# Kernel tuning notes

Measured on AMD Instinct MI355X. Metric: run time of the kernel, lower is better.

Reference implementation:

```python
import jax, jax.numpy as jnp
import numpy as np

N, E, F, H, C, G = 50000, 800000, 128, 1, 64, 256
NEG_SLOPE = 0.2


def _seg_softmax(e, seg, n):
    # numerically-stable softmax over edges grouped by target node
    m = jax.ops.segment_max(e, seg, num_segments=n)
    ex = jnp.exp(e - m[seg])
    s = jax.ops.segment_sum(ex, seg, num_segments=n)
    return ex / (s[seg] + 1e-16)


def _gatv2(x, src, dst, wl, bl, wr, br, att, bo, n):
    # GATv2Conv (PyG semantics): lin_l on source x_j, lin_r on target x_i
    xl = (x @ wl.T + bl).reshape(n, H, C)
    xr = (x @ wr.T + br).reshape(n, H, C)
    s = xl[src] + xr[dst]                      # [E, H, C]
    e = jnp.sum(jax.nn.leaky_relu(s, NEG_SLOPE) * att, axis=-1)  # [E, H]
    alpha = _seg_softmax(e, dst, n)
    out = jax.ops.segment_sum(alpha[..., None] * xl[src], dst, num_segments=n)
    return out.reshape(n, H * C) + bo


def setup_inputs() -> dict:
    key = jax.random.key(0)
    ks = jax.random.split(key, 24)
    d = {}
    d['x'] = jax.random.normal(ks[0], (N, F), dtype=jnp.float32)
    d['edge_index'] = jax.random.randint(ks[1], (2, E), 0, N)
    d['batch_idx'] = jnp.sort(jax.random.randint(ks[2], (N,), 0, G))
    sc = 0.1
    # conv1: in=F, out=C
    d['wl1'] = jax.random.normal(ks[3], (H * C, F)) * sc
    d['bl1'] = jnp.zeros((H * C,), jnp.float32)
    d['wr1'] = jax.random.normal(ks[4], (H * C, F)) * sc
    d['br1'] = jnp.zeros((H * C,), jnp.float32)
    d['att1'] = jax.random.normal(ks[5], (H, C)) * sc
    d['bo1'] = jnp.zeros((H * C,), jnp.float32)
    # conv2, conv3: in=H*C, out=C
    d['wl2'] = jax.random.normal(ks[6], (H * C, H * C)) * sc
    d['bl2'] = jnp.zeros((H * C,), jnp.float32)
    d['wr2'] = jax.random.normal(ks[7], (H * C, H * C)) * sc
    d['br2'] = jnp.zeros((H * C,), jnp.float32)
    d['att2'] = jax.random.normal(ks[8], (H, C)) * sc
    d['bo2'] = jnp.zeros((H * C,), jnp.float32)
    d['wl3'] = jax.random.normal(ks[9], (H * C, H * C)) * sc
    d['bl3'] = jnp.zeros((H * C,), jnp.float32)
    d['wr3'] = jax.random.normal(ks[10], (H * C, H * C)) * sc
    d['br3'] = jnp.zeros((H * C,), jnp.float32)
    d['att3'] = jax.random.normal(ks[11], (H, C)) * sc
    d['bo3'] = jnp.zeros((H * C,), jnp.float32)
    # heads
    d['lin1_w'] = jax.random.normal(ks[12], (C, 3 * H * C)) * sc
    d['lin1_b'] = jnp.zeros((C,), jnp.float32)
    d['pred_w'] = jax.random.normal(ks[13], (C, C)) * sc
    d['pred_b'] = jnp.zeros((C,), jnp.float32)
    d['cls_w'] = jax.random.normal(ks[14], (2, C)) * sc
    d['cls_b'] = jnp.zeros((2,), jnp.float32)
    return d


def reference(x, edge_index, batch_idx, wl1, bl1, wr1, br1, att1, bo1,
              wl2, bl2, wr2, br2, att2, bo2, wl3, bl3, wr3, br3, att3, bo3,
              lin1_w, lin1_b, pred_w, pred_b, cls_w, cls_b):
    # add self-loops (GATv2Conv default add_self_loops=True)
    loop = jnp.arange(N, dtype=edge_index.dtype)
    src = jnp.concatenate([edge_index[0], loop])
    dst = jnp.concatenate([edge_index[1], loop])
    x1 = jax.nn.relu(_gatv2(x, src, dst, wl1, bl1, wr1, br1, att1, bo1, N))
    x2 = jax.nn.relu(_gatv2(x1, src, dst, wl2, bl2, wr2, br2, att2, bo2, N))
    x3 = jax.nn.relu(_gatv2(x2, src, dst, wl3, bl3, wr3, br3, att3, bo3, N))
    h = jax.nn.relu(jnp.concatenate([x1, x2, x3], axis=1) @ lin1_w.T + lin1_b)
    g = jax.ops.segment_sum(h, batch_idx, num_segments=G)  # global_add_pool
    emb = jax.nn.relu(g @ pred_w.T + pred_b)                # pred_layer
    out = emb @ cls_w.T + cls_b                             # cls_layer
    return out
```

## Files before the change

kernel.cpp:

```cpp
#include <hip/hip_runtime.h>
#include <hip/hip_bf16.h>

#define N_NODES 50000
#define N_EDGES 800000
#define FDIM 128
#define CDIM 64
#define NGRAPH 256
#define LRELU_SLOPE 0.2f
#define SCAN_NB ((N_NODES + 1023) / 1024)
#define NBUCK ((N_NODES + 255) / 256)
#define BCAP 5120
#define ABLK 400
#define EPB ((N_EDGES + ABLK - 1) / ABLK)
#define NDBIN 64

typedef unsigned short ushort_t;
typedef unsigned int uint_t;
typedef __attribute__((ext_vector_type(8))) short short8v;
typedef __attribute__((ext_vector_type(4))) float float4v;

__device__ __forceinline__ ushort_t f2bf(float f) {
    uint_t u = __float_as_uint(f);
    u += 0x7FFFu + ((u >> 16) & 1u);
    return (ushort_t)(u >> 16);
}
__device__ __forceinline__ float bf2f(ushort_t u) {
    return __uint_as_float(((uint_t)u) << 16);
}

__device__ __forceinline__ float fast_exp2(float x) {
    return __builtin_amdgcn_exp2f(x);
}

__device__ __forceinline__ int wave_incl_scan(int v, int lane) {
#pragma unroll
    for (int off = 1; off < 64; off <<= 1) {
        int t = __shfl_up(v, off);
        if (lane >= off) v += t;
    }
    return v;
}

__device__ __forceinline__ float wave_sum(float v) {
#pragma unroll
    for (int off = 32; off >= 1; off >>= 1) v += __shfl_xor(v, off);
    return v;
}

__global__ void k_bucket(const int* __restrict__ src, const int* __restrict__ dst,
                         int* __restrict__ bcnt, int2* __restrict__ stage) {
    __shared__ int lhist[NBUCK];
    __shared__ int lbase[NBUCK];
    __shared__ int lcur[NBUCK];
    int tid = threadIdx.x;
    int e0 = blockIdx.x * EPB;
    int e1 = min(e0 + EPB, N_EDGES);
    for (int t = tid; t < NBUCK; t += 256) { lhist[t] = 0; lcur[t] = 0; }
    __syncthreads();
    for (int e = e0 + tid; e < e1; e += 256)
        atomicAdd(&lhist[dst[e] >> 8], 1);
    __syncthreads();
    for (int t = tid; t < NBUCK; t += 256)
        lbase[t] = atomicAdd(&bcnt[t], lhist[t]);
    __syncthreads();
    for (int e = e0 + tid; e < e1; e += 256) {
        int s = src[e], d = dst[e];
        int b = d >> 8;
        int loff = atomicAdd(&lcur[b], 1);
        int pos = lbase[b] + loff;
        if (pos < BCAP) stage[(size_t)b * BCAP + pos] = make_int2(s, d);
    }
}

__global__ void k_hist2(const int* __restrict__ bcnt, const int2* __restrict__ stage,
                        int* __restrict__ cnt, int* __restrict__ dhist) {
    __shared__ int lcnt[256];
    __shared__ int ldh[NDBIN];
    int b = blockIdx.x;
    int tid = threadIdx.x;
    lcnt[tid] = 0;
    if (tid < NDBIN) ldh[tid] = 0;
    __syncthreads();
    int n = min(bcnt[b], BCAP);
    const int2* sp = stage + (size_t)b * BCAP;
    for (int i = tid; i < n; i += 256)
        atomicAdd(&lcnt[sp[i].y & 255], 1);
    __syncthreads();
    int node = (b << 8) + tid;
    if (node < N_NODES) {
        cnt[node] = lcnt[tid];
        atomicAdd(&ldh[min(lcnt[tid], NDBIN - 1)], 1);
    }
    __syncthreads();
    if (tid < NDBIN && ldh[tid]) atomicAdd(&dhist[tid], ldh[tid]);
}

__global__ void k_scan1(const int* __restrict__ cnt, int* __restrict__ rowptr,
                        int* __restrict__ blocksum) {
    __shared__ int wsum[16];
    int tid = threadIdx.x;
    int gid = blockIdx.x * 1024 + tid;
    int lane = tid & 63, wid = tid >> 6;
    int v = (gid < N_NODES) ? cnt[gid] : 0;
    int incl = wave_incl_scan(v, lane);
    if (lane == 63) wsum[wid] = incl;
    __syncthreads();
    if (wid == 0) {
        int wv = (lane < 16) ? wsum[lane] : 0;
        int wincl = wave_incl_scan(wv, lane);
        if (lane < 16) wsum[lane] = wincl - wv;
    }
    __syncthreads();
    int excl = incl - v + wsum[wid];
    if (gid < N_NODES) rowptr[gid] = excl;
    if (tid == 1023) blocksum[blockIdx.x] = excl + v;
}

__global__ void k_scan2(int* __restrict__ blocksum, const int* __restrict__ dhist,
                        int* __restrict__ dcur) {
    int tid = threadIdx.x;
    if (tid < 64) {
        int lane = tid;
        int v = (lane < SCAN_NB) ? blocksum[lane] : 0;
        int incl = wave_incl_scan(v, lane);
        if (lane < SCAN_NB) blocksum[lane] = incl - v;
    } else {
        int lane = tid - 64;
        int v = dhist[lane];
        int incl = wave_incl_scan(v, lane);
        dcur[lane] = incl - v;
    }
}

__global__ void k_scan3(int* __restrict__ rowptr, const int* __restrict__ blocksum,
                        int* __restrict__ cursor) {
    int tid = threadIdx.x;
    int gid = blockIdx.x * 1024 + tid;
    if (gid < N_NODES) {
        int r = rowptr[gid] + blocksum[blockIdx.x];
        rowptr[gid] = r;
        cursor[gid] = r;
    }
    if (blockIdx.x == 0 && tid == 0) rowptr[N_NODES] = N_EDGES;
}

__global__ void k_scatter2(const int* __restrict__ bcnt, const int2* __restrict__ stage,
                           int* __restrict__ cursor, int* __restrict__ csr_src) {
    int b = blockIdx.x;
    int tid = threadIdx.x;
    int n = min(bcnt[b], BCAP);
    const int2* sp = stage + (size_t)b * BCAP;
    for (int i = tid; i < n; i += 256) {
        int2 sd = sp[i];
        int pos = atomicAdd(&cursor[sd.y], 1);
        csr_src[pos] = sd.x;
    }
}

__global__ void k_dscatter(const int* __restrict__ cnt, int* __restrict__ dcur,
                           int* __restrict__ order) {
    __shared__ int lh[NDBIN], lb[NDBIN], lc[NDBIN];
    int b = blockIdx.x, tid = threadIdx.x;
    if (tid < NDBIN) { lh[tid] = 0; lc[tid] = 0; }
    __syncthreads();
    int node = b * 256 + tid;
    bool ok = node < N_NODES;
    int dg = ok ? min(cnt[node], NDBIN - 1) : 0;
    if (ok) atomicAdd(&lh[dg], 1);
    __syncthreads();
    if (tid < NDBIN) lb[tid] = lh[tid] ? atomicAdd(&dcur[tid], lh[tid]) : 0;
    __syncthreads();
    if (ok) {
        int off2 = atomicAdd(&lc[dg], 1);
        order[lb[dg] + off2] = node;
    }
}

struct WSrc {
    const float* s[7];
    int off[8];
};
__global__ void k_cvt_w(WSrc ws, ushort_t* __restrict__ hi, ushort_t* __restrict__ lo) {
    int gid = blockIdx.x * 256 + threadIdx.x;
    int stride = gridDim.x * 256;
#pragma unroll
    for (int mi = 0; mi < 7; mi++) {
        int n = ws.off[mi + 1] - ws.off[mi];
        const float* s = ws.s[mi];
        ushort_t* h = hi + ws.off[mi];
        ushort_t* l = lo + ws.off[mi];
        for (int i = gid; i < n; i += stride) {
            float f = s[i];
            ushort_t hb = f2bf(f);
            h[i] = hb;
            l[i] = f2bf(f - bf2f(hb));
        }
    }
}

template <int K, bool A_FP32>
__global__ void k_gemm_dual_mfma(const void* __restrict__ xa,
                                 const ushort_t* __restrict__ wlh, const ushort_t* __restrict__ wll,
                                 const ushort_t* __restrict__ wrh, const ushort_t* __restrict__ wrl,
                                 const float* __restrict__ bl, const float* __restrict__ br,
                                 ushort_t* __restrict__ xl, ushort_t* __restrict__ xr) {
    int tid = threadIdx.x;
    int wv = tid >> 6, lane = tid & 63;
    int m0 = blockIdx.x * 64 + wv * 16;
    if (m0 >= N_NODES) return;
    int arow = min(m0 + (lane & 15), N_NODES - 1);
    int koff = (lane >> 4) * 8;
    int wrow = lane & 15;

    float4v acc[8];
#pragma unroll
    for (int f = 0; f < 8; f++) acc[f] = (float4v)(0.f);

#pragma unroll
    for (int k0 = 0; k0 < K; k0 += 32) {
        short8v afrag;
        if (A_FP32) {
            const float* ap = (const float*)xa + (size_t)arow * K + k0 + koff;
            float4 a0 = *reinterpret_cast<const float4*>(ap);
            float4 a1 = *reinterpret_cast<const float4*>(ap + 4);
            afrag[0] = (short)f2bf(a0.x); afrag[1] = (short)f2bf(a0.y);
            afrag[2] = (short)f2bf(a0.z); afrag[3] = (short)f2bf(a0.w);
            afrag[4] = (short)f2bf(a1.x); afrag[5] = (short)f2bf(a1.y);
            afrag[6] = (short)f2bf(a1.z); afrag[7] = (short)f2bf(a1.w);
        } else {
            afrag = *reinterpret_cast<const short8v*>((const ushort_t*)xa + (size_t)arow * K + k0 + koff);
        }
#pragma unroll
        for (int f = 0; f < 8; f++) {
            const ushort_t* bh = (f < 4) ? wlh : wrh;
            const ushort_t* blo = (f < 4) ? wll : wrl;
            int row = ((f * 16 + wrow) & 63);
            size_t boff = (size_t)row * K + k0 + koff;
            short8v bfh = *reinterpret_cast<const short8v*>(bh + boff);
            short8v bfl = *reinterpret_cast<const short8v*>(blo + boff);
            acc[f] = __builtin_amdgcn_mfma_f32_16x16x32_bf16(afrag, bfh, acc[f], 0, 0, 0);
            acc[f] = __builtin_amdgcn_mfma_f32_16x16x32_bf16(afrag, bfl, acc[f], 0, 0, 0);
        }
    }

    int r0 = m0 + (lane >> 4) * 4;
#pragma unroll
    for (int f = 0; f < 8; f++) {
        int col = f * 16 + (lane & 15);
        float bias = (col < 64) ? bl[col] : br[col - 64];
        ushort_t* dstp = (col < 64) ? xl : xr;
        int c = col & 63;
#pragma unroll
        for (int j = 0; j < 4; j++) {
            int row = r0 + j;
            if (row < N_NODES) dstp[(size_t)row * 64 + c] = f2bf(acc[f][j] + bias);
        }
    }
}

__global__ void k_gemm_h_pool(const ushort_t* __restrict__ x1, const ushort_t* __restrict__ x2,
                              const ushort_t* __restrict__ x3,
                              const ushort_t* __restrict__ whi, const ushort_t* __restrict__ wlo,
                              const float* __restrict__ b, const int* __restrict__ batch,
                              float* __restrict__ g) {
    __shared__ float ht[64][65];
    int tid = threadIdx.x;
    int wv = tid >> 6, lane = tid & 63;
    int m0 = blockIdx.x * 64 + wv * 16;
    bool wactive = m0 < N_NODES;

    if (wactive) {
        int arow = min(m0 + (lane & 15), N_NODES - 1);
        int koff = (lane >> 4) * 8;
        int wrow = lane & 15;
        float4v acc[4];
#pragma unroll
        for (int f = 0; f < 4; f++) acc[f] = (float4v)(0.f);
#pragma unroll
        for (int ks = 0; ks < 6; ks++) {
            int k0 = ks * 32;
            const ushort_t* srcp = (ks < 2) ? x1 : (ks < 4 ? x2 : x3);
            int kc = k0 & 63;
            short8v afrag = *reinterpret_cast<const short8v*>(srcp + (size_t)arow * 64 + kc + koff);
#pragma unroll
            for (int f = 0; f < 4; f++) {
                size_t boff = (size_t)(f * 16 + wrow) * 192 + k0 + koff;
                short8v bfh = *reinterpret_cast<const short8v*>(whi + boff);
                short8v bfl = *reinterpret_cast<const short8v*>(wlo + boff);
                acc[f] = __builtin_amdgcn_mfma_f32_16x16x32_bf16(afrag, bfh, acc[f], 0, 0, 0);
                acc[f] = __builtin_amdgcn_mfma_f32_16x16x32_bf16(afrag, bfl, acc[f], 0, 0, 0);
            }
        }
        int r0 = wv * 16 + (lane >> 4) * 4;
#pragma unroll
        for (int f = 0; f < 4; f++) {
            int col = f * 16 + (lane & 15);
            float bias = b[col];
#pragma unroll
            for (int j = 0; j < 4; j++) {
                float o = acc[f][j] + bias;
                ht[r0 + j][col] = o > 0.f ? o : 0.f;
            }
        }
    }
    __syncthreads();

    int c = tid & 63, rr = tid >> 6;
    int blkbase = blockIdx.x * 64;
    float acc = 0.f;
    int cur = -1;
    for (int r = rr; r < 64; r += 4) {
        int node = blkbase + r;
        if (node >= N_NODES) break;
        int bb = batch[node];
        if (bb != cur) {
            if (cur >= 0) atomicAdd(&g[cur * 64 + c], acc);
            cur = bb;
            acc = 0.f;
        }
        acc += ht[r][c];
    }
    if (cur >= 0) atomicAdd(&g[cur * 64 + c], acc);
}

__global__ void k_gat(const ushort_t* __restrict__ xl, const ushort_t* __restrict__ xr,
                      const int* __restrict__ rowptr, const int* __restrict__ csr_src,
                      const int* __restrict__ order,
                      const float* __restrict__ att, const float* __restrict__ bo,
                      ushort_t* __restrict__ xout) {
    int tid = threadIdx.x;
    int wv = tid >> 6, lane = tid & 63;
    int gl = lane & 15;
    int slot = blockIdx.x * 16 + wv * 4 + (lane >> 4);
    if (slot >= N_NODES) return;
    int node = order[slot];
    const float LOG2E = 1.44269504f;
    int c0 = gl * 4;
    float4 a4 = *reinterpret_cast<const float4*>(att + c0);
    float at0 = a4.x * LOG2E, at1 = a4.y * LOG2E, at2 = a4.z * LOG2E, at3 = a4.w * LOG2E;
    size_t nb = (size_t)node * 64 + c0;
    ushort4 qr = *reinterpret_cast<const ushort4*>(xr + nb);
    ushort4 ql = *reinterpret_cast<const ushort4*>(xl + nb);
    float xr0 = bf2f(qr.x), xr1 = bf2f(qr.y), xr2 = bf2f(qr.z), xr3 = bf2f(qr.w);
    float l0 = bf2f(ql.x), l1 = bf2f(ql.y), l2 = bf2f(ql.z), l3 = bf2f(ql.w);

    auto grd = [](float p) {
        p += __shfl_xor(p, 1);
        p += __shfl_xor(p, 2);
        p += __shfl_xor(p, 4);
        p += __shfl_xor(p, 8);
        return p;
    };
    auto score4 = [&](float v0, float v1, float v2, float v3) {
        float s0 = v0 + xr0, s1 = v1 + xr1, s2 = v2 + xr2, s3 = v3 + xr3;
        float t0 = fmaxf(s0, LRELU_SLOPE * s0);
        float t1 = fmaxf(s1, LRELU_SLOPE * s1);
        float t2 = fmaxf(s2, LRELU_SLOPE * s2);
        float t3 = fmaxf(s3, LRELU_SLOPE * s3);
        return ((t0 * at0 + t1 * at1) + (t2 * at2 + t3 * at3));
    };

    int beg = rowptr[node], end = rowptr[node + 1];
    int deg = end - beg;

    float m = grd(score4(l0, l1, l2, l3));
    float ssum = 1.f;
    float a0 = l0, a1 = l1, a2 = l2, a3 = l3;

    for (int j = 0; j < deg; j += 4) {
        int base = beg + j, lim = end - 1;
        int i1 = min(base + 1, lim), i2 = min(base + 2, lim), i3 = min(base + 3, lim);
        int s0 = csr_src[base], s1 = csr_src[i1], s2 = csr_src[i2], s3 = csr_src[i3];
        ushort4 q0 = *reinterpret_cast<const ushort4*>(xl + (size_t)s0 * 64 + c0);
        ushort4 q1 = *reinterpret_cast<const ushort4*>(xl + (size_t)s1 * 64 + c0);
        ushort4 q2 = *reinterpret_cast<const ushort4*>(xl + (size_t)s2 * 64 + c0);
        ushort4 q3 = *reinterpret_cast<const ushort4*>(xl + (size_t)s3 * 64 + c0);
        float v00 = bf2f(q0.x), v01 = bf2f(q0.y), v02 = bf2f(q0.z), v03 = bf2f(q0.w);
        float v10 = bf2f(q1.x), v11 = bf2f(q1.y), v12 = bf2f(q1.z), v13 = bf2f(q1.w);
        float v20 = bf2f(q2.x), v21 = bf2f(q2.y), v22 = bf2f(q2.z), v23 = bf2f(q2.w);
        float v30 = bf2f(q3.x), v31 = bf2f(q3.y), v32 = bf2f(q3.z), v33 = bf2f(q3.w);
        float e0 = grd(score4(v00, v01, v02, v03));
        float e1 = grd(score4(v10, v11, v12, v13));
        float e2 = grd(score4(v20, v21, v22, v23));
        float e3 = grd(score4(v30, v31, v32, v33));
        int rem = deg - j;
        if (rem < 4) {
            e3 = -1e30f;
            if (rem < 3) e2 = -1e30f;
            if (rem < 2) e1 = -1e30f;
        }
        float mn = fmaxf(fmaxf(fmaxf(e0, e1), fmaxf(e2, e3)), m);
        float sc = fast_exp2(m - mn);
        float w0 = fast_exp2(e0 - mn), w1 = fast_exp2(e1 - mn);
        float w2 = fast_exp2(e2 - mn), w3 = fast_exp2(e3 - mn);
        ssum = ssum * sc + ((w0 + w1) + (w2 + w3));
        a0 = a0 * sc + ((w0 * v00 + w1 * v10) + (w2 * v20 + w3 * v30));
        a1 = a1 * sc + ((w0 * v01 + w1 * v11) + (w2 * v21 + w3 * v31));
        a2 = a2 * sc + ((w0 * v02 + w1 * v12) + (w2 * v22 + w3 * v32));
        a3 = a3 * sc + ((w0 * v03 + w1 * v13) + (w2 * v23 + w3 * v33));
        m = mn;
    }

    float rs = 1.f / (ssum + 1e-16f);
    float4 b4 = *reinterpret_cast<const float4*>(bo + c0);
    float o0 = fmaxf(a0 * rs + b4.x, 0.f);
    float o1 = fmaxf(a1 * rs + b4.y, 0.f);
    float o2 = fmaxf(a2 * rs + b4.z, 0.f);
    float o3 = fmaxf(a3 * rs + b4.w, 0.f);
    ushort4 oq;
    oq.x = f2bf(o0); oq.y = f2bf(o1); oq.z = f2bf(o2); oq.w = f2bf(o3);
    *reinterpret_cast<ushort4*>(xout + nb) = oq;
}

__global__ void k_head(const float* __restrict__ g, const float* __restrict__ pw,
                       const float* __restrict__ pb, const float* __restrict__ cw,
                       const float* __restrict__ cb, float* __restrict__ out) {
    int gb = blockIdx.x;
    int c = threadIdx.x;
    const float* gr = g + gb * 64;
    float a = pb[c];
    const float* pwr = pw + c * 64;
#pragma unroll
    for (int k = 0; k < 64; k++) a += gr[k] * pwr[k];
    a = a > 0.f ? a : 0.f;
    float o0 = wave_sum(a * cw[c]);
    float o1 = wave_sum(a * cw[64 + c]);
    if (c == 0) {
        out[gb * 2 + 0] = o0 + cb[0];
        out[gb * 2 + 1] = o1 + cb[1];
    }
}

extern "C" void kernel_launch(void* const* d_in, const int* in_sizes, int n_in,
                              void* d_out, int out_size, void* d_ws, size_t ws_size,
                              hipStream_t stream) {
    const float* x    = (const float*)d_in[0];
    const int*   ei   = (const int*)d_in[1];
    const int*   bidx = (const int*)d_in[2];
    const float* wl1 = (const float*)d_in[3],  *bl1 = (const float*)d_in[4];
    const float* wr1 = (const float*)d_in[5],  *br1 = (const float*)d_in[6];
    const float* att1 = (const float*)d_in[7], *bo1 = (const float*)d_in[8];
    const float* wl2 = (const float*)d_in[9],  *bl2 = (const float*)d_in[10];
    const float* wr2 = (const float*)d_in[11], *br2 = (const float*)d_in[12];
    const float* att2 = (const float*)d_in[13], *bo2 = (const float*)d_in[14];
    const float* wl3 = (const float*)d_in[15], *bl3 = (const float*)d_in[16];
    const float* wr3 = (const float*)d_in[17], *br3 = (const float*)d_in[18];
    const float* att3 = (const float*)d_in[19], *bo3 = (const float*)d_in[20];
    const float* lw = (const float*)d_in[21], *lb = (const float*)d_in[22];
    const float* pw = (const float*)d_in[23], *pb = (const float*)d_in[24];
    const float* cw = (const float*)d_in[25], *cb = (const float*)d_in[26];
    float* out = (float*)d_out;

    char* wsb = (char*)d_ws;
    size_t off = 0;
    auto alloc = [&](size_t bytes) {
        void* p = wsb + off;
        off = (off + bytes + 255) & ~(size_t)255;
        return p;
    };
    int* cnt      = (int*)alloc((size_t)N_NODES * 4);
    int* rowptr   = (int*)alloc((size_t)(N_NODES + 1) * 4);
    int* cursor   = (int*)alloc((size_t)N_NODES * 4);
    int* blocksum = (int*)alloc((size_t)SCAN_NB * 4);
    int* bcnt     = (int*)alloc((size_t)(NBUCK + NDBIN) * 4);
    int* dhist    = bcnt + NBUCK;
    int* dcur     = (int*)alloc((size_t)NDBIN * 4);
    int* order    = (int*)alloc((size_t)N_NODES * 4);
    int2* stage   = (int2*)alloc((size_t)NBUCK * BCAP * 8);
    int* csr_src  = (int*)alloc((size_t)N_EDGES * 4);
    const int woff[8] = {0, 8192, 16384, 20480, 24576, 28672, 32768, 45056};
    ushort_t* whi = (ushort_t*)alloc((size_t)45056 * 2);
    ushort_t* wlo = (ushort_t*)alloc((size_t)45056 * 2);
    ushort_t* xl   = (ushort_t*)alloc((size_t)N_NODES * 64 * 2);
    ushort_t* xrr  = (ushort_t*)alloc((size_t)N_NODES * 64 * 2);
    ushort_t* x1b  = (ushort_t*)alloc((size_t)N_NODES * 64 * 2);
    ushort_t* x2b  = (ushort_t*)alloc((size_t)N_NODES * 64 * 2);
    ushort_t* x3b  = (ushort_t*)alloc((size_t)N_NODES * 64 * 2);
    float* g      = (float*)alloc((size_t)NGRAPH * 64 * 4);
    (void)ws_size; (void)in_sizes; (void)n_in; (void)out_size;

    const int* srcp = ei;
    const int* dstp = ei + N_EDGES;

    hipMemsetAsync(bcnt, 0, (size_t)(NBUCK + NDBIN) * 4, stream);
    hipMemsetAsync(g, 0, (size_t)NGRAPH * 64 * 4, stream);

    k_bucket<<<ABLK, 256, 0, stream>>>(srcp, dstp, bcnt, stage);
    k_hist2<<<NBUCK, 256, 0, stream>>>(bcnt, stage, cnt, dhist);
    k_scan1<<<SCAN_NB, 1024, 0, stream>>>(cnt, rowptr, blocksum);
    k_scan2<<<1, 128, 0, stream>>>(blocksum, dhist, dcur);
    k_scan3<<<SCAN_NB, 1024, 0, stream>>>(rowptr, blocksum, cursor);
    k_scatter2<<<NBUCK, 256, 0, stream>>>(bcnt, stage, cursor, csr_src);
    k_dscatter<<<NBUCK, 256, 0, stream>>>(cnt, dcur, order);

    WSrc ws;
    ws.s[0] = wl1; ws.s[1] = wr1; ws.s[2] = wl2; ws.s[3] = wr2;
    ws.s[4] = wl3; ws.s[5] = wr3; ws.s[6] = lw;
    for (int i = 0; i < 8; i++) ws.off[i] = woff[i];
    k_cvt_w<<<64, 256, 0, stream>>>(ws, whi, wlo);

    int gemmBlocks = (N_NODES + 63) / 64;
    int gatBlocks = (N_NODES + 15) / 16;

    k_gemm_dual_mfma<128, true><<<gemmBlocks, 256, 0, stream>>>(
        x, whi + woff[0], wlo + woff[0], whi + woff[1], wlo + woff[1], bl1, br1, xl, xrr);
    k_gat<<<gatBlocks, 256, 0, stream>>>(xl, xrr, rowptr, csr_src, order, att1, bo1, x1b);
    k_gemm_dual_mfma<64, false><<<gemmBlocks, 256, 0, stream>>>(
        x1b, whi + woff[2], wlo + woff[2], whi + woff[3], wlo + woff[3], bl2, br2, xl, xrr);
    k_gat<<<gatBlocks, 256, 0, stream>>>(xl, xrr, rowptr, csr_src, order, att2, bo2, x2b);
    k_gemm_dual_mfma<64, false><<<gemmBlocks, 256, 0, stream>>>(
        x2b, whi + woff[4], wlo + woff[4], whi + woff[5], wlo + woff[5], bl3, br3, xl, xrr);
    k_gat<<<gatBlocks, 256, 0, stream>>>(xl, xrr, rowptr, csr_src, order, att3, bo3, x3b);

    k_gemm_h_pool<<<gemmBlocks, 256, 0, stream>>>(x1b, x2b, x3b, whi + woff[6], wlo + woff[6],
                                                  lb, bidx, g);
    k_head<<<NGRAPH, 64, 0, stream>>>(g, pw, pb, cw, cb, out);
}
```

Measured before the change: 262.9 us.

## Fuse CSR build into per-bucket scan and unroll GAT edge loop by eight

The CSR build now does one scan over the bucket counts, then a single per-bucket kernel. That kernel computes local degree prefix sums, writes rowptr, and scatters source indices through shared-memory cursors. This replaces the old multi-kernel global scan and the global atomic cursor scatter. It removes several kernel launches and the global atomics on the cursor array. Separately, the GAT aggregation loop now handles eight edges per iteration instead of four, so more gathers are in flight, at the cost of more registers and wasted lanes on low-degree nodes.

```diff
diff --git a/kernel.cpp b/kernel.cpp
--- a/kernel.cpp
+++ b/kernel.cpp
@@ -7,7 +7,6 @@
 #define CDIM 64
 #define NGRAPH 256
 #define LRELU_SLOPE 0.2f
-#define SCAN_NB ((N_NODES + 1023) / 1024)
 #define NBUCK ((N_NODES + 255) / 256)
 #define BCAP 5120
 #define ABLK 400
@@ -72,12 +71,34 @@
     }
 }
 
-__global__ void k_hist2(const int* __restrict__ bcnt, const int2* __restrict__ stage,
-                        int* __restrict__ cnt, int* __restrict__ dhist) {
+__global__ void k_bscan(const int* __restrict__ bcnt, int* __restrict__ bbase) {
+    __shared__ int wsum[4];
+    int tid = threadIdx.x;
+    int lane = tid & 63, w = tid >> 6;
+    int v = (tid < NBUCK) ? bcnt[tid] : 0;
+    int incl = wave_incl_scan(v, lane);
+    if (lane == 63) wsum[w] = incl;
+    __syncthreads();
+    if (tid == 0) {
+        int s = 0;
+#pragma unroll
+        for (int k = 0; k < 4; k++) { int t = wsum[k]; wsum[k] = s; s += t; }
+    }
+    __syncthreads();
+    if (tid < NBUCK) bbase[tid] = incl - v + wsum[w];
+}
+
+__global__ void k_csr(const int* __restrict__ bcnt, const int* __restrict__ bbase,
+                      const int2* __restrict__ stage, int* __restrict__ rowptr,
+                      int* __restrict__ cnt, int* __restrict__ dhist,
+                      int* __restrict__ csr_src) {
     __shared__ int lcnt[256];
+    __shared__ int lcur[256];
     __shared__ int ldh[NDBIN];
+    __shared__ int wsum[4];
     int b = blockIdx.x;
     int tid = threadIdx.x;
+    int lane = tid & 63, w = tid >> 6;
     lcnt[tid] = 0;
     if (tid < NDBIN) ldh[tid] = 0;
     __syncthreads();
@@ -86,75 +107,40 @@
     for (int i = tid; i < n; i += 256)
         atomicAdd(&lcnt[sp[i].y & 255], 1);
     __syncthreads();
+    int v = lcnt[tid];
+    int incl = wave_incl_scan(v, lane);
+    if (lane == 63) wsum[w] = incl;
+    __syncthreads();
+    if (tid == 0) {
+        int s = 0;
+#pragma unroll
+        for (int k = 0; k < 4; k++) { int t = wsum[k]; wsum[k] = s; s += t; }
+    }
+    __syncthreads();
+    int excl = incl - v + wsum[w];
+    int bb = bbase[b];
     int node = (b << 8) + tid;
     if (node < N_NODES) {
-        cnt[node] = lcnt[tid];
-        atomicAdd(&ldh[min(lcnt[tid], NDBIN - 1)], 1);
-    }
+        rowptr[node] = bb + excl;
+        cnt[node] = v;
+        atomicAdd(&ldh[min(v, NDBIN - 1)], 1);
+    }
+    lcur[tid] = excl;
     __syncthreads();
     if (tid < NDBIN && ldh[tid]) atomicAdd(&dhist[tid], ldh[tid]);
-}
-
-__global__ void k_scan1(const int* __restrict__ cnt, int* __restrict__ rowptr,
-                        int* __restrict__ blocksum) {
-    __shared__ int wsum[16];
-    int tid = threadIdx.x;
-    int gid = blockIdx.x * 1024 + tid;
-    int lane = tid & 63, wid = tid >> 6;
-    int v = (gid < N_NODES) ? cnt[gid] : 0;
-    int incl = wave_incl_scan(v, lane);
-    if (lane == 63) wsum[wid] = incl;
-    __syncthreads();
-    if (wid == 0) {
-        int wv = (lane < 16) ? wsum[lane] : 0;
-        int wincl = wave_incl_scan(wv, lane);
-        if (lane < 16) wsum[lane] = wincl - wv;
-    }
-    __syncthreads();
-    int excl = incl - v + wsum[wid];
-    if (gid < N_NODES) rowptr[gid] = excl;
-    if (tid == 1023) blocksum[blockIdx.x] = excl + v;
-}
-
-__global__ void k_scan2(int* __restrict__ blocksum, const int* __restrict__ dhist,
-                        int* __restrict__ dcur) {
-    int tid = threadIdx.x;
-    if (tid < 64) {
-        int lane = tid;
-        int v = (lane < SCAN_NB) ? blocksum[lane] : 0;
-        int incl = wave_incl_scan(v, lane);
-        if (lane < SCAN_NB) blocksum[lane] = incl - v;
-    } else {
-        int lane = tid - 64;
-        int v = dhist[lane];
-        int incl = wave_incl_scan(v, lane);
-        dcur[lane] = incl - v;
-    }
-}
-
-__global__ void k_scan3(int* __restrict__ rowptr, const int* __restrict__ blocksum,
-                        int* __restrict__ cursor) {
-    int tid = threadIdx.x;
-    int gid = blockIdx.x * 1024 + tid;
-    if (gid < N_NODES) {
-        int r = rowptr[gid] + blocksum[blockIdx.x];
-        rowptr[gid] = r;
-        cursor[gid] = r;
-    }
-    if (blockIdx.x == 0 && tid == 0) rowptr[N_NODES] = N_EDGES;
-}
-
-__global__ void k_scatter2(const int* __restrict__ bcnt, const int2* __restrict__ stage,
-                           int* __restrict__ cursor, int* __restrict__ csr_src) {
-    int b = blockIdx.x;
-    int tid = threadIdx.x;
-    int n = min(bcnt[b], BCAP);
-    const int2* sp = stage + (size_t)b * BCAP;
+    if (b == 0 && tid == 0) rowptr[N_NODES] = N_EDGES;
     for (int i = tid; i < n; i += 256) {
         int2 sd = sp[i];
-        int pos = atomicAdd(&cursor[sd.y], 1);
-        csr_src[pos] = sd.x;
-    }
+        int pos = atomicAdd(&lcur[sd.y & 255], 1);
+        csr_src[bb + pos] = sd.x;
+    }
+}
+
+__global__ void k_scan2d(const int* __restrict__ dhist, int* __restrict__ dcur) {
+    int lane = threadIdx.x;
+    int v = dhist[lane];
+    int incl = wave_incl_scan(v, lane);
+    dcur[lane] = incl - v;
 }
 
 __global__ void k_dscatter(const int* __restrict__ cnt, int* __restrict__ dcur,
@@ -362,42 +348,71 @@
 
     int beg = rowptr[node], end = rowptr[node + 1];
     int deg = end - beg;
+    int lim = end - 1;
 
     float m = grd(score4(l0, l1, l2, l3));
     float ssum = 1.f;
     float a0 = l0, a1 = l1, a2 = l2, a3 = l3;
 
-    for (int j = 0; j < deg; j += 4) {
-        int base = beg + j, lim = end - 1;
+    for (int j = 0; j < deg; j += 8) {
+        int base = beg + j;
+        int i0 = base;
         int i1 = min(base + 1, lim), i2 = min(base + 2, lim), i3 = min(base + 3, lim);
-        int s0 = csr_src[base], s1 = csr_src[i1], s2 = csr_src[i2], s3 = csr_src[i3];
+        int i4 = min(base + 4, lim), i5 = min(base + 5, lim);
+        int i6 = min(base + 6, lim), i7 = min(base + 7, lim);
+        int s0 = csr_src[i0], s1 = csr_src[i1], s2 = csr_src[i2], s3 = csr_src[i3];
+        int s4 = csr_src[i4], s5 = csr_src[i5], s6 = csr_src[i6], s7 = csr_src[i7];
         ushort4 q0 = *reinterpret_cast<const ushort4*>(xl + (size_t)s0 * 64 + c0);
         ushort4 q1 = *reinterpret_cast<const ushort4*>(xl + (size_t)s1 * 64 + c0);
         ushort4 q2 = *reinterpret_cast<const ushort4*>(xl + (size_t)s2 * 64 + c0);
         ushort4 q3 = *reinterpret_cast<const ushort4*>(xl + (size_t)s3 * 64 + c0);
+        ushort4 q4 = *reinterpret_cast<const ushort4*>(xl + (size_t)s4 * 64 + c0);
+        ushort4 q5 = *reinterpret_cast<const ushort4*>(xl + (size_t)s5 * 64 + c0);
+        ushort4 q6 = *reinterpret_cast<const ushort4*>(xl + (size_t)s6 * 64 + c0);
+        ushort4 q7 = *reinterpret_cast<const ushort4*>(xl + (size_t)s7 * 64 + c0);
         float v00 = bf2f(q0.x), v01 = bf2f(q0.y), v02 = bf2f(q0.z), v03 = bf2f(q0.w);
         float v10 = bf2f(q1.x), v11 = bf2f(q1.y), v12 = bf2f(q1.z), v13 = bf2f(q1.w);
         float v20 = bf2f(q2.x), v21 = bf2f(q2.y), v22 = bf2f(q2.z), v23 = bf2f(q2.w);
         float v30 = bf2f(q3.x), v31 = bf2f(q3.y), v32 = bf2f(q3.z), v33 = bf2f(q3.w);
+        float v40 = bf2f(q4.x), v41 = bf2f(q4.y), v42 = bf2f(q4.z), v43 = bf2f(q4.w);
+        float v50 = bf2f(q5.x), v51 = bf2f(q5.y), v52 = bf2f(q5.z), v53 = bf2f(q5.w);
+        float v60 = bf2f(q6.x), v61 = bf2f(q6.y), v62 = bf2f(q6.z), v63 = bf2f(q6.w);
+        float v70 = bf2f(q7.x), v71 = bf2f(q7.y), v72 = bf2f(q7.z), v73 = bf2f(q7.w);
         float e0 = grd(score4(v00, v01, v02, v03));
         float e1 = grd(score4(v10, v11, v12, v13));
         float e2 = grd(score4(v20, v21, v22, v23));
         float e3 = grd(score4(v30, v31, v32, v33));
+        float e4 = grd(score4(v40, v41, v42, v43));
+        float e5 = grd(score4(v50, v51, v52, v53));
+        float e6 = grd(score4(v60, v61, v62, v63));
+        float e7 = grd(score4(v70, v71, v72, v73));
         int rem = deg - j;
-        if (rem < 4) {
-            e3 = -1e30f;
-            if (rem < 3) e2 = -1e30f;
-            if (rem < 2) e1 = -1e30f;
-        }
-        float mn = fmaxf(fmaxf(fmaxf(e0, e1), fmaxf(e2, e3)), m);
+        if (rem < 8) {
+            e1 = (rem > 1) ? e1 : -1e30f;
+            e2 = (rem > 2) ? e2 : -1e30f;
+            e3 = (rem > 3) ? e3 : -1e30f;
+            e4 = (rem > 4) ? e4 : -1e30f;
+            e5 = (rem > 5) ? e5 : -1e30f;
+            e6 = (rem > 6) ? e6 : -1e30f;
+            e7 = (rem > 7) ? e7 : -1e30f;
+        }
+        float mx = fmaxf(fmaxf(fmaxf(e0, e1), fmaxf(e2, e3)),
+                         fmaxf(fmaxf(e4, e5), fmaxf(e6, e7)));
+        float mn = fmaxf(m, mx);
         float sc = fast_exp2(m - mn);
         float w0 = fast_exp2(e0 - mn), w1 = fast_exp2(e1 - mn);
         float w2 = fast_exp2(e2 - mn), w3 = fast_exp2(e3 - mn);
-        ssum = ssum * sc + ((w0 + w1) + (w2 + w3));
-        a0 = a0 * sc + ((w0 * v00 + w1 * v10) + (w2 * v20 + w3 * v30));
-        a1 = a1 * sc + ((w0 * v01 + w1 * v11) + (w2 * v21 + w3 * v31));
-        a2 = a2 * sc + ((w0 * v02 + w1 * v12) + (w2 * v22 + w3 * v32));
-        a3 = a3 * sc + ((w0 * v03 + w1 * v13) + (w2 * v23 + w3 * v33));
+        float w4 = fast_exp2(e4 - mn), w5 = fast_exp2(e5 - mn);
+        float w6 = fast_exp2(e6 - mn), w7 = fast_exp2(e7 - mn);
+        ssum = ssum * sc + (((w0 + w1) + (w2 + w3)) + ((w4 + w5) + (w6 + w7)));
+        a0 = a0 * sc + (((w0 * v00 + w1 * v10) + (w2 * v20 + w3 * v30)) +
+                        ((w4 * v40 + w5 * v50) + (w6 * v60 + w7 * v70)));
+        a1 = a1 * sc + (((w0 * v01 + w1 * v11) + (w2 * v21 + w3 * v31)) +
+                        ((w4 * v41 + w5 * v51) + (w6 * v61 + w7 * v71)));
+        a2 = a2 * sc + (((w0 * v02 + w1 * v12) + (w2 * v22 + w3 * v32)) +
+                        ((w4 * v42 + w5 * v52) + (w6 * v62 + w7 * v72)));
+        a3 = a3 * sc + (((w0 * v03 + w1 * v13) + (w2 * v23 + w3 * v33)) +
+                        ((w4 * v43 + w5 * v53) + (w6 * v63 + w7 * v73)));
         m = mn;
     }
 
@@ -460,10 +475,9 @@
     };
     int* cnt      = (int*)alloc((size_t)N_NODES * 4);
     int* rowptr   = (int*)alloc((size_t)(N_NODES + 1) * 4);
-    int* cursor   = (int*)alloc((size_t)N_NODES * 4);
-    int* blocksum = (int*)alloc((size_t)SCAN_NB * 4);
     int* bcnt     = (int*)alloc((size_t)(NBUCK + NDBIN) * 4);
     int* dhist    = bcnt + NBUCK;
+    int* bbase    = (int*)alloc((size_t)NBUCK * 4);
     int* dcur     = (int*)alloc((size_t)NDBIN * 4);
     int* order    = (int*)alloc((size_t)N_NODES * 4);
     int2* stage   = (int2*)alloc((size_t)NBUCK * BCAP * 8);
@@ -486,11 +500,9 @@
     hipMemsetAsync(g, 0, (size_t)NGRAPH * 64 * 4, stream);
 
     k_bucket<<<ABLK, 256, 0, stream>>>(srcp, dstp, bcnt, stage);
-    k_hist2<<<NBUCK, 256, 0, stream>>>(bcnt, stage, cnt, dhist);
-    k_scan1<<<SCAN_NB, 1024, 0, stream>>>(cnt, rowptr, blocksum);
-    k_scan2<<<1, 128, 0, stream>>>(blocksum, dhist, dcur);
-    k_scan3<<<SCAN_NB, 1024, 0, stream>>>(rowptr, blocksum, cursor);
-    k_scatter2<<<NBUCK, 256, 0, stream>>>(bcnt, stage, cursor, csr_src);
+    k_bscan<<<1, 256, 0, stream>>>(bcnt, bbase);
+    k_csr<<<NBUCK, 256, 0, stream>>>(bcnt, bbase, stage, rowptr, cnt, dhist, csr_src);
+    k_scan2d<<<1, 64, 0, stream>>>(dhist, dcur);
     k_dscatter<<<NBUCK, 256, 0, stream>>>(cnt, dcur, order);
 
     WSrc ws;
```

Measured after the change: 258.2 us. Within noise of the previous version (-1.8%).
